# Kernel optimization log

Hardware: AMD Instinct MI355X
Metric: run time of the kernel (lower is better)

## Reference

```python
import jax, jax.numpy as jnp
import numpy as np

HIDDEN = 1024
NUM_HEADS = 16
HEAD_SIZE = HIDDEN // NUM_HEADS


def setup_inputs() -> dict:
    key = jax.random.key(0)
    k1, k2, k3 = jax.random.split(key, 3)
    B, S = 2, 2048
    x = jax.random.normal(k1, (B, S, HIDDEN), dtype=jnp.float32)
    # query projection (source reuses it for both q and k)
    Wq = jax.random.normal(k2, (HIDDEN, HIDDEN), dtype=jnp.float32) / np.sqrt(HIDDEN)
    bq = jax.random.normal(k3, (HIDDEN,), dtype=jnp.float32) * 0.01
    return {"x": x, "Wq": Wq, "bq": bq}


def reference(x, Wq, bq):
    B, S, _ = x.shape
    # NOTE: source bug-for-bug: k uses the query projection too
    q = x @ Wq + bq                      # [B,S,D]
    k = x @ Wq + bq                      # [B,S,D]
    q = q.reshape(B, S, NUM_HEADS, HEAD_SIZE)
    k = k.reshape(B, S, NUM_HEADS, HEAD_SIZE)
    # scores: [B,H,S,S]
    e = jnp.einsum("bqhd,bkhd->bhqk", q, k)
    s = jax.nn.softmax(e / jnp.sqrt(jnp.float32(HEAD_SIZE)), axis=-1)
    return s
```

## Files before the change

### kernel.cpp

```cpp
#include <hip/hip_runtime.h>

#define HIDDEN 1024
#define SEQ 2048
#define NB 2
#define PSTRIDE 2052
#define NT 16

typedef _Float16 half8 __attribute__((ext_vector_type(8)));
typedef _Float16 half4 __attribute__((ext_vector_type(4)));
typedef float f32x4 __attribute__((ext_vector_type(4)));

#define GL2LDS(gp, lp) __builtin_amdgcn_global_load_lds( \
    (const __attribute__((address_space(1))) void*)(gp), \
    (__attribute__((address_space(3))) void*)(lp), 16, 0, 0)

__global__ __launch_bounds__(256) void cast_wt(const float* __restrict__ w,
                                               _Float16* __restrict__ wt) {
    __shared__ float tile[32][33];
    int bx = blockIdx.x * 32, by = blockIdx.y * 32;
    int tx = threadIdx.x, ty = threadIdx.y;
    #pragma unroll
    for (int i = 0; i < 32; i += 8)
        tile[ty + i][tx] = w[(by + ty + i) * HIDDEN + bx + tx];
    __syncthreads();
    #pragma unroll
    for (int i = 0; i < 32; i += 8)
        wt[(bx + ty + i) * HIDDEN + by + tx] = (_Float16)tile[tx][ty + i];
}

__global__ __launch_bounds__(512) void proj_gemm(const float* __restrict__ X,
                                                 const _Float16* __restrict__ Bt,
                                                 const float* __restrict__ bias,
                                                 _Float16* __restrict__ Q) {
    __shared__ _Float16 As[128 * 64];
    __shared__ _Float16 Bs[128 * 64];
    const int m0 = blockIdx.x * 128;
    const int n0 = blockIdx.y * 128;
    const int tid = threadIdx.x;
    const int w = tid >> 6, l = tid & 63;
    const int wm = w >> 2, wn = w & 3;
    const int lrow = l & 15, lkslot = l >> 4;

    const int srow = l >> 3, sslot = l & 7;

    f32x4 acc[4][2] = {};

    for (int k0 = 0; k0 < HIDDEN; k0 += 64) {
        __syncthreads();
        #pragma unroll
        for (int j = 0; j < 2; ++j) {
            const int chunk = w * 2 + j;
            const int r = chunk * 8 + srow;
            const int gslot = sslot ^ (r & 7);
            GL2LDS(&Bt[(size_t)(n0 + r) * HIDDEN + k0 + gslot * 8], Bs + chunk * 512);
        }
        #pragma unroll
        for (int it = 0; it < 2; ++it) {
            const int id = it * 512 + tid;
            const int row = id >> 3, slot = id & 7;
            const float* src = &X[(size_t)(m0 + row) * HIDDEN + k0 + slot * 8];
            f32x4 v0 = *(const f32x4*)src;
            f32x4 v1 = *(const f32x4*)(src + 4);
            half8 hv;
            hv[0] = (_Float16)v0[0]; hv[1] = (_Float16)v0[1];
            hv[2] = (_Float16)v0[2]; hv[3] = (_Float16)v0[3];
            hv[4] = (_Float16)v1[0]; hv[5] = (_Float16)v1[1];
            hv[6] = (_Float16)v1[2]; hv[7] = (_Float16)v1[3];
            *(half8*)&As[row * 64 + (slot ^ (row & 7)) * 8] = hv;
        }
        __syncthreads();
        #pragma unroll
        for (int kk = 0; kk < 64; kk += 32) {
            const int csb = kk >> 3;
            half8 af[4], bf[2];
            #pragma unroll
            for (int m = 0; m < 4; ++m) {
                const int R = wm * 64 + m * 16 + lrow;
                const int slot = (csb + lkslot) ^ (R & 7);
                af[m] = *(const half8*)&As[R * 64 + slot * 8];
            }
            #pragma unroll
            for (int n = 0; n < 2; ++n) {
                const int R = wn * 32 + n * 16 + lrow;
                const int slot = (csb + lkslot) ^ (R & 7);
                bf[n] = *(const half8*)&Bs[R * 64 + slot * 8];
            }
            #pragma unroll
            for (int m = 0; m < 4; ++m)
                #pragma unroll
                for (int n = 0; n < 2; ++n)
                    acc[m][n] = __builtin_amdgcn_mfma_f32_16x16x32_f16(af[m], bf[n], acc[m][n], 0, 0, 0);
        }
    }
    const int lr4 = (l >> 4) * 4, lc = l & 15;
    #pragma unroll
    for (int n = 0; n < 2; ++n) {
        int gcol = n0 + wn * 32 + n * 16 + lc;
        float b = bias[gcol];
        #pragma unroll
        for (int m = 0; m < 4; ++m) {
            #pragma unroll
            for (int r = 0; r < 4; ++r) {
                int grow = m0 + wm * 64 + m * 16 + lr4 + r;
                Q[(size_t)grow * HIDDEN + gcol] = (_Float16)(acc[m][n][r] + b);
            }
        }
    }
}

__global__ __launch_bounds__(1024, 4) void scores_softmax(const _Float16* __restrict__ Qh,
                                                          float* __restrict__ out) {
    __shared__ __align__(16) _Float16 p[2][16][PSTRIDE];
    __shared__ float rsum_lds[2][8][16];

    const int raw = blockIdx.x;
    const int xcd = raw & 7, i = raw >> 3;
    const int bh = xcd * 4 + (i >> 3);
    const int qchunk = i & 7;
    const int b = bh >> 4, h = bh & 15;

    const int tid = threadIdx.x;
    const int wv = tid >> 6;
    const int l = tid & 63;
    const int lq = l & 15, lg = l >> 4;
    const int hoff = h * 64;
    const _Float16* qbase = Qh + (size_t)b * SEQ * HIDDEN;
    const size_t outbase = (size_t)(b * 16 + h) * SEQ * SEQ;

    if (wv < 8) {
        const int pw = wv;
        const _Float16* kbase = qbase + (size_t)(pw * 256 + lq) * HIDDEN + hoff + lg * 8;
        for (int t = 0; t <= NT; ++t) {
            if (t < NT) {
                const int buf = t & 1;
                const int q0 = qchunk * 256 + t * 16;
                const _Float16* qp = qbase + (size_t)(q0 + lq) * HIDDEN + hoff + lg * 8;
                const half8 bq0 = *(const half8*)qp;
                const half8 bq1 = *(const half8*)(qp + 32);
                float rsum = 0.f;
                #pragma unroll
                for (int s = 0; s < 16; ++s) {
                    const _Float16* a = kbase + (size_t)s * 16 * HIDDEN;
                    half8 ka = *(const half8*)a;
                    half8 kb = *(const half8*)(a + 32);
                    f32x4 acc = {};
                    acc = __builtin_amdgcn_mfma_f32_16x16x32_f16(ka, bq0, acc, 0, 0, 0);
                    acc = __builtin_amdgcn_mfma_f32_16x16x32_f16(kb, bq1, acc, 0, 0, 0);
                    float e0 = exp2f(fmaf(acc[0], 0.18033688011f, -11.54156033f));
                    float e1 = exp2f(fmaf(acc[1], 0.18033688011f, -11.54156033f));
                    float e2 = exp2f(fmaf(acc[2], 0.18033688011f, -11.54156033f));
                    float e3 = exp2f(fmaf(acc[3], 0.18033688011f, -11.54156033f));
                    rsum += (e0 + e1) + (e2 + e3);
                    half4 hv;
                    hv[0] = (_Float16)e0; hv[1] = (_Float16)e1;
                    hv[2] = (_Float16)e2; hv[3] = (_Float16)e3;
                    *(half4*)&p[buf][lq][pw * 256 + s * 16 + lg * 4] = hv;
                }
                rsum += __shfl_xor(rsum, 16);
                rsum += __shfl_xor(rsum, 32);
                if (l < 16) rsum_lds[buf][pw][l] = rsum;
            }
            asm volatile("s_waitcnt lgkmcnt(0)" ::: "memory");
            __builtin_amdgcn_s_barrier();
        }
    } else {
        const int cw = wv - 8;
        for (int t = 0; t <= NT; ++t) {
            if (t > 0) {
                const int pbuf = (t - 1) & 1;
                #pragma unroll
                for (int rr = 0; rr < 2; ++rr) {
                    const int r = cw * 2 + rr;
                    float rs = 0.f;
                    #pragma unroll
                    for (int w8 = 0; w8 < 8; ++w8) rs += rsum_lds[pbuf][w8][r];
                    const float rinv = 1.0f / rs;
                    float* orow = out + outbase
                                + (size_t)(qchunk * 256 + (t - 1) * 16 + r) * SEQ;
                    #pragma unroll
                    for (int ii = 0; ii < 8; ++ii) {
                        half4 hv = *(const half4*)&p[pbuf][r][ii * 256 + l * 4];
                        f32x4 v;
                        v[0] = (float)hv[0] * rinv; v[1] = (float)hv[1] * rinv;
                        v[2] = (float)hv[2] * rinv; v[3] = (float)hv[3] * rinv;
                        __builtin_nontemporal_store(v, (f32x4*)(orow + ii * 256 + l * 4));
                    }
                }
            }
            asm volatile("s_waitcnt lgkmcnt(0)" ::: "memory");
            __builtin_amdgcn_s_barrier();
        }
    }
}

extern "C" void kernel_launch(void* const* d_in, const int* in_sizes, int n_in,
                              void* d_out, int out_size, void* d_ws, size_t ws_size,
                              hipStream_t stream) {
    const float* x  = (const float*)d_in[0];
    const float* Wq = (const float*)d_in[1];
    const float* bq = (const float*)d_in[2];
    float* out = (float*)d_out;

    _Float16* qh = (_Float16*)d_ws;
    _Float16* wt = qh + (size_t)4 * 1024 * 1024;

    cast_wt<<<dim3(32, 32), dim3(32, 8), 0, stream>>>(Wq, wt);
    proj_gemm<<<dim3(NB * SEQ / 128, HIDDEN / 128), 512, 0, stream>>>(x, wt, bq, qh);
    scores_softmax<<<256, 1024, 0, stream>>>(qh, out);
}
```

Baseline: 131.4 us.

## Double-buffer projection GEMM tiles and remap blocks for XCD-local reuse

The projection GEMM now keeps two LDS buffers for its A and B tiles. The next k-slice is fetched into registers (X) and LDS (W via global_load_lds) while MFMAs run on the current slice, so global load latency overlaps compute and there is one barrier per iteration instead of two. The grid is flattened to 256 blocks, and the block index is remapped so blocks on the same XCD share M tiles and reuse X in L2. The cost is double the LDS and extra live registers for the prefetched fp32 X values.

```diff
diff --git a/kernel.cpp b/kernel.cpp
--- a/kernel.cpp
+++ b/kernel.cpp
@@ -32,10 +32,13 @@
                                                  const _Float16* __restrict__ Bt,
                                                  const float* __restrict__ bias,
                                                  _Float16* __restrict__ Q) {
-    __shared__ _Float16 As[128 * 64];
-    __shared__ _Float16 Bs[128 * 64];
-    const int m0 = blockIdx.x * 128;
-    const int n0 = blockIdx.y * 128;
+    __shared__ _Float16 As[2][128 * 64];
+    __shared__ _Float16 Bs[2][128 * 64];
+    const int raw = blockIdx.x;
+    const int xcd = raw & 7, j = raw >> 3;
+    const int mt = xcd * 4 + (j >> 3);
+    const int ntile = j & 7;
+    const int m0 = mt * 128, n0 = ntile * 128;
     const int tid = threadIdx.x;
     const int w = tid >> 6, l = tid & 63;
     const int wm = w >> 2, wn = w & 3;
@@ -43,32 +46,60 @@
 
     const int srow = l >> 3, sslot = l & 7;
 
+    f32x4 av[2][2];
+
     f32x4 acc[4][2] = {};
 
-    for (int k0 = 0; k0 < HIDDEN; k0 += 64) {
-        __syncthreads();
-        #pragma unroll
-        for (int j = 0; j < 2; ++j) {
-            const int chunk = w * 2 + j;
+    {
+        #pragma unroll
+        for (int j2 = 0; j2 < 2; ++j2) {
+            const int chunk = w * 2 + j2;
             const int r = chunk * 8 + srow;
             const int gslot = sslot ^ (r & 7);
-            GL2LDS(&Bt[(size_t)(n0 + r) * HIDDEN + k0 + gslot * 8], Bs + chunk * 512);
+            GL2LDS(&Bt[(size_t)(n0 + r) * HIDDEN + gslot * 8], &Bs[0][chunk * 512]);
         }
         #pragma unroll
         for (int it = 0; it < 2; ++it) {
             const int id = it * 512 + tid;
             const int row = id >> 3, slot = id & 7;
-            const float* src = &X[(size_t)(m0 + row) * HIDDEN + k0 + slot * 8];
-            f32x4 v0 = *(const f32x4*)src;
-            f32x4 v1 = *(const f32x4*)(src + 4);
+            const float* src = &X[(size_t)(m0 + row) * HIDDEN + slot * 8];
+            av[it][0] = *(const f32x4*)src;
+            av[it][1] = *(const f32x4*)(src + 4);
+        }
+        #pragma unroll
+        for (int it = 0; it < 2; ++it) {
+            const int id = it * 512 + tid;
+            const int row = id >> 3, slot = id & 7;
             half8 hv;
-            hv[0] = (_Float16)v0[0]; hv[1] = (_Float16)v0[1];
-            hv[2] = (_Float16)v0[2]; hv[3] = (_Float16)v0[3];
-            hv[4] = (_Float16)v1[0]; hv[5] = (_Float16)v1[1];
-            hv[6] = (_Float16)v1[2]; hv[7] = (_Float16)v1[3];
-            *(half8*)&As[row * 64 + (slot ^ (row & 7)) * 8] = hv;
+            hv[0] = (_Float16)av[it][0][0]; hv[1] = (_Float16)av[it][0][1];
+            hv[2] = (_Float16)av[it][0][2]; hv[3] = (_Float16)av[it][0][3];
+            hv[4] = (_Float16)av[it][1][0]; hv[5] = (_Float16)av[it][1][1];
+            hv[6] = (_Float16)av[it][1][2]; hv[7] = (_Float16)av[it][1][3];
+            *(half8*)&As[0][row * 64 + (slot ^ (row & 7)) * 8] = hv;
         }
         __syncthreads();
+    }
+
+    for (int t = 0; t < 16; ++t) {
+        const int cur = t & 1, nxt = cur ^ 1;
+        const int k1 = (t + 1) * 64;
+        if (t < 15) {
+            #pragma unroll
+            for (int j2 = 0; j2 < 2; ++j2) {
+                const int chunk = w * 2 + j2;
+                const int r = chunk * 8 + srow;
+                const int gslot = sslot ^ (r & 7);
+                GL2LDS(&Bt[(size_t)(n0 + r) * HIDDEN + k1 + gslot * 8], &Bs[nxt][chunk * 512]);
+            }
+            #pragma unroll
+            for (int it = 0; it < 2; ++it) {
+                const int id = it * 512 + tid;
+                const int row = id >> 3, slot = id & 7;
+                const float* src = &X[(size_t)(m0 + row) * HIDDEN + k1 + slot * 8];
+                av[it][0] = *(const f32x4*)src;
+                av[it][1] = *(const f32x4*)(src + 4);
+            }
+        }
         #pragma unroll
         for (int kk = 0; kk < 64; kk += 32) {
             const int csb = kk >> 3;
@@ -77,13 +108,13 @@
             for (int m = 0; m < 4; ++m) {
                 const int R = wm * 64 + m * 16 + lrow;
                 const int slot = (csb + lkslot) ^ (R & 7);
-                af[m] = *(const half8*)&As[R * 64 + slot * 8];
+                af[m] = *(const half8*)&As[cur][R * 64 + slot * 8];
             }
             #pragma unroll
             for (int n = 0; n < 2; ++n) {
                 const int R = wn * 32 + n * 16 + lrow;
                 const int slot = (csb + lkslot) ^ (R & 7);
-                bf[n] = *(const half8*)&Bs[R * 64 + slot * 8];
+                bf[n] = *(const half8*)&Bs[cur][R * 64 + slot * 8];
             }
             #pragma unroll
             for (int m = 0; m < 4; ++m)
@@ -91,7 +122,22 @@
                 for (int n = 0; n < 2; ++n)
                     acc[m][n] = __builtin_amdgcn_mfma_f32_16x16x32_f16(af[m], bf[n], acc[m][n], 0, 0, 0);
         }
-    }
+        if (t < 15) {
+            #pragma unroll
+            for (int it = 0; it < 2; ++it) {
+                const int id = it * 512 + tid;
+                const int row = id >> 3, slot = id & 7;
+                half8 hv;
+                hv[0] = (_Float16)av[it][0][0]; hv[1] = (_Float16)av[it][0][1];
+                hv[2] = (_Float16)av[it][0][2]; hv[3] = (_Float16)av[it][0][3];
+                hv[4] = (_Float16)av[it][1][0]; hv[5] = (_Float16)av[it][1][1];
+                hv[6] = (_Float16)av[it][1][2]; hv[7] = (_Float16)av[it][1][3];
+                *(half8*)&As[nxt][row * 64 + (slot ^ (row & 7)) * 8] = hv;
+            }
+        }
+        __syncthreads();
+    }
+
     const int lr4 = (l >> 4) * 4, lc = l & 15;
     #pragma unroll
     for (int n = 0; n < 2; ++n) {
@@ -205,6 +251,6 @@
     _Float16* wt = qh + (size_t)4 * 1024 * 1024;
 
     cast_wt<<<dim3(32, 32), dim3(32, 8), 0, stream>>>(Wq, wt);
-    proj_gemm<<<dim3(NB * SEQ / 128, HIDDEN / 128), 512, 0, stream>>>(x, wt, bq, qh);
+    proj_gemm<<<256, 512, 0, stream>>>(x, wt, bq, qh);
     scores_softmax<<<256, 1024, 0, stream>>>(qh, out);
 }
```

Result: no change. 133.1 us (+1.3%).

## Replace producer/consumer LDS softmax with register-resident per-block scores

Applied to the files above, without the earlier changes.

The scores/softmax kernel drops the warp-specialized producer/consumer scheme, where 8 waves computed exp scores into a double-buffered LDS tile and 8 other waves normalized and stored them. Each 256-thread block now handles 16 query rows. Each wave keeps its 512 columns of fp16 exponentials in registers and software-prefetches the next K fragment. Row sums are combined through a tiny LDS array with a single barrier. This removes the large LDS footprint and the per-tile barriers, and gives many more small blocks for occupancy, at the cost of high register pressure (32 half4 values per thread) and no overlap between computing scores and storing them within a block.

```diff
diff --git a/kernel.cpp b/kernel.cpp
--- a/kernel.cpp
+++ b/kernel.cpp
@@ -3,8 +3,6 @@
 #define HIDDEN 1024
 #define SEQ 2048
 #define NB 2
-#define PSTRIDE 2052
-#define NT 16
 
 typedef _Float16 half8 __attribute__((ext_vector_type(8)));
 typedef _Float16 half4 __attribute__((ext_vector_type(4)));
@@ -108,88 +106,74 @@
     }
 }
 
-__global__ __launch_bounds__(1024, 4) void scores_softmax(const _Float16* __restrict__ Qh,
-                                                          float* __restrict__ out) {
-    __shared__ __align__(16) _Float16 p[2][16][PSTRIDE];
-    __shared__ float rsum_lds[2][8][16];
+__global__ __launch_bounds__(256) void scores_softmax(const _Float16* __restrict__ Qh,
+                                                      float* __restrict__ out) {
+    __shared__ float rsum_lds[4][16];
 
     const int raw = blockIdx.x;
-    const int xcd = raw & 7, i = raw >> 3;
-    const int bh = xcd * 4 + (i >> 3);
-    const int qchunk = i & 7;
+    const int bid = (raw & 7) * 512 + (raw >> 3);
+    const int bh = bid >> 7;
+    const int qb = bid & 127;
     const int b = bh >> 4, h = bh & 15;
 
     const int tid = threadIdx.x;
-    const int wv = tid >> 6;
+    const int w = tid >> 6;
     const int l = tid & 63;
     const int lq = l & 15, lg = l >> 4;
+    const int q0 = qb * 16;
     const int hoff = h * 64;
     const _Float16* qbase = Qh + (size_t)b * SEQ * HIDDEN;
-    const size_t outbase = (size_t)(b * 16 + h) * SEQ * SEQ;
 
-    if (wv < 8) {
-        const int pw = wv;
-        const _Float16* kbase = qbase + (size_t)(pw * 256 + lq) * HIDDEN + hoff + lg * 8;
-        for (int t = 0; t <= NT; ++t) {
-            if (t < NT) {
-                const int buf = t & 1;
-                const int q0 = qchunk * 256 + t * 16;
-                const _Float16* qp = qbase + (size_t)(q0 + lq) * HIDDEN + hoff + lg * 8;
-                const half8 bq0 = *(const half8*)qp;
-                const half8 bq1 = *(const half8*)(qp + 32);
-                float rsum = 0.f;
-                #pragma unroll
-                for (int s = 0; s < 16; ++s) {
-                    const _Float16* a = kbase + (size_t)s * 16 * HIDDEN;
-                    half8 ka = *(const half8*)a;
-                    half8 kb = *(const half8*)(a + 32);
-                    f32x4 acc = {};
-                    acc = __builtin_amdgcn_mfma_f32_16x16x32_f16(ka, bq0, acc, 0, 0, 0);
-                    acc = __builtin_amdgcn_mfma_f32_16x16x32_f16(kb, bq1, acc, 0, 0, 0);
-                    float e0 = exp2f(fmaf(acc[0], 0.18033688011f, -11.54156033f));
-                    float e1 = exp2f(fmaf(acc[1], 0.18033688011f, -11.54156033f));
-                    float e2 = exp2f(fmaf(acc[2], 0.18033688011f, -11.54156033f));
-                    float e3 = exp2f(fmaf(acc[3], 0.18033688011f, -11.54156033f));
-                    rsum += (e0 + e1) + (e2 + e3);
-                    half4 hv;
-                    hv[0] = (_Float16)e0; hv[1] = (_Float16)e1;
-                    hv[2] = (_Float16)e2; hv[3] = (_Float16)e3;
-                    *(half4*)&p[buf][lq][pw * 256 + s * 16 + lg * 4] = hv;
-                }
-                rsum += __shfl_xor(rsum, 16);
-                rsum += __shfl_xor(rsum, 32);
-                if (l < 16) rsum_lds[buf][pw][l] = rsum;
-            }
-            asm volatile("s_waitcnt lgkmcnt(0)" ::: "memory");
-            __builtin_amdgcn_s_barrier();
-        }
-    } else {
-        const int cw = wv - 8;
-        for (int t = 0; t <= NT; ++t) {
-            if (t > 0) {
-                const int pbuf = (t - 1) & 1;
-                #pragma unroll
-                for (int rr = 0; rr < 2; ++rr) {
-                    const int r = cw * 2 + rr;
-                    float rs = 0.f;
-                    #pragma unroll
-                    for (int w8 = 0; w8 < 8; ++w8) rs += rsum_lds[pbuf][w8][r];
-                    const float rinv = 1.0f / rs;
-                    float* orow = out + outbase
-                                + (size_t)(qchunk * 256 + (t - 1) * 16 + r) * SEQ;
-                    #pragma unroll
-                    for (int ii = 0; ii < 8; ++ii) {
-                        half4 hv = *(const half4*)&p[pbuf][r][ii * 256 + l * 4];
-                        f32x4 v;
-                        v[0] = (float)hv[0] * rinv; v[1] = (float)hv[1] * rinv;
-                        v[2] = (float)hv[2] * rinv; v[3] = (float)hv[3] * rinv;
-                        __builtin_nontemporal_store(v, (f32x4*)(orow + ii * 256 + l * 4));
-                    }
-                }
-            }
-            asm volatile("s_waitcnt lgkmcnt(0)" ::: "memory");
-            __builtin_amdgcn_s_barrier();
-        }
+    const _Float16* qp = qbase + (size_t)(q0 + lq) * HIDDEN + hoff + lg * 8;
+    const half8 bq0 = *(const half8*)qp;
+    const half8 bq1 = *(const half8*)(qp + 32);
+
+    const _Float16* kbase = qbase + (size_t)(w * 512 + lq) * HIDDEN + hoff + lg * 8;
+
+    half4 pv[32];
+    float rsum = 0.f;
+
+    half8 ka = *(const half8*)kbase;
+    half8 kb = *(const half8*)(kbase + 32);
+    #pragma unroll
+    for (int s = 0; s < 32; ++s) {
+        const int sn = (s < 31) ? s + 1 : 0;
+        const _Float16* a = kbase + (size_t)sn * 16 * HIDDEN;
+        half8 na = *(const half8*)a;
+        half8 nb = *(const half8*)(a + 32);
+
+        f32x4 acc = {};
+        acc = __builtin_amdgcn_mfma_f32_16x16x32_f16(ka, bq0, acc, 0, 0, 0);
+        acc = __builtin_amdgcn_mfma_f32_16x16x32_f16(kb, bq1, acc, 0, 0, 0);
+        float e0 = exp2f(fmaf(acc[0], 0.18033688011f, -11.54156033f));
+        float e1 = exp2f(fmaf(acc[1], 0.18033688011f, -11.54156033f));
+        float e2 = exp2f(fmaf(acc[2], 0.18033688011f, -11.54156033f));
+        float e3 = exp2f(fmaf(acc[3], 0.18033688011f, -11.54156033f));
+        rsum += (e0 + e1) + (e2 + e3);
+        half4 hv;
+        hv[0] = (_Float16)e0; hv[1] = (_Float16)e1;
+        hv[2] = (_Float16)e2; hv[3] = (_Float16)e3;
+        pv[s] = hv;
+        ka = na; kb = nb;
+    }
+
+    rsum += __shfl_xor(rsum, 16);
+    rsum += __shfl_xor(rsum, 32);
+    if (l < 16) rsum_lds[w][l] = rsum;
+    __syncthreads();
+    const float rs = rsum_lds[0][lq] + rsum_lds[1][lq] + rsum_lds[2][lq] + rsum_lds[3][lq];
+    const float rinv = 1.0f / rs;
+
+    float* orow = out + (size_t)(b * 16 + h) * SEQ * SEQ
+                      + (size_t)(q0 + lq) * SEQ + w * 512 + lg * 4;
+    #pragma unroll
+    for (int s = 0; s < 32; ++s) {
+        f32x4 v;
+        v[0] = (float)pv[s][0] * rinv;
+        v[1] = (float)pv[s][1] * rinv;
+        v[2] = (float)pv[s][2] * rinv;
+        v[3] = (float)pv[s][3] * rinv;
+        __builtin_nontemporal_store(v, (f32x4*)(orow + s * 16));
     }
 }
 
@@ -206,5 +190,5 @@
 
     cast_wt<<<dim3(32, 32), dim3(32, 8), 0, stream>>>(Wq, wt);
     proj_gemm<<<dim3(NB * SEQ / 128, HIDDEN / 128), 512, 0, stream>>>(x, wt, bq, qh);
-    scores_softmax<<<256, 1024, 0, stream>>>(qh, out);
+    scores_softmax<<<NB * 16 * (SEQ / 16), 256, 0, stream>>>(qh, out);
 }
```

New measurement: 259.5 us. 1.97x slower.

## Unify producer/consumer waves and keep K fragments resident in registers

Applied to the files above, without the earlier changes.

The kernel no longer splits into 8 score-computing waves and 8 store waves. All 16 waves now compute scores for a 128-key slice and then each normalizes and streams out one query row, with one barrier per tile. Each wave's K fragments are loaded once into registers and reused across all 16 query tiles, which removes the repeated global K loads, and the next Q tile is prefetched after the barrier. The trade is that compute and stores no longer overlap across waves, register pressure rises without the occupancy hint, and one buffer could be overwritten early since only a single barrier separates writes of buf from the reads two iterations later.

```diff
diff --git a/kernel.cpp b/kernel.cpp
--- a/kernel.cpp
+++ b/kernel.cpp
@@ -108,10 +108,10 @@
     }
 }
 
-__global__ __launch_bounds__(1024, 4) void scores_softmax(const _Float16* __restrict__ Qh,
-                                                          float* __restrict__ out) {
+__global__ __launch_bounds__(1024) void scores_softmax(const _Float16* __restrict__ Qh,
+                                                       float* __restrict__ out) {
     __shared__ __align__(16) _Float16 p[2][16][PSTRIDE];
-    __shared__ float rsum_lds[2][8][16];
+    __shared__ float rsum_lds[2][16][16];
 
     const int raw = blockIdx.x;
     const int xcd = raw & 7, i = raw >> 3;
@@ -127,68 +127,64 @@
     const _Float16* qbase = Qh + (size_t)b * SEQ * HIDDEN;
     const size_t outbase = (size_t)(b * 16 + h) * SEQ * SEQ;
 
-    if (wv < 8) {
-        const int pw = wv;
-        const _Float16* kbase = qbase + (size_t)(pw * 256 + lq) * HIDDEN + hoff + lg * 8;
-        for (int t = 0; t <= NT; ++t) {
-            if (t < NT) {
-                const int buf = t & 1;
-                const int q0 = qchunk * 256 + t * 16;
-                const _Float16* qp = qbase + (size_t)(q0 + lq) * HIDDEN + hoff + lg * 8;
-                const half8 bq0 = *(const half8*)qp;
-                const half8 bq1 = *(const half8*)(qp + 32);
-                float rsum = 0.f;
-                #pragma unroll
-                for (int s = 0; s < 16; ++s) {
-                    const _Float16* a = kbase + (size_t)s * 16 * HIDDEN;
-                    half8 ka = *(const half8*)a;
-                    half8 kb = *(const half8*)(a + 32);
-                    f32x4 acc = {};
-                    acc = __builtin_amdgcn_mfma_f32_16x16x32_f16(ka, bq0, acc, 0, 0, 0);
-                    acc = __builtin_amdgcn_mfma_f32_16x16x32_f16(kb, bq1, acc, 0, 0, 0);
-                    float e0 = exp2f(fmaf(acc[0], 0.18033688011f, -11.54156033f));
-                    float e1 = exp2f(fmaf(acc[1], 0.18033688011f, -11.54156033f));
-                    float e2 = exp2f(fmaf(acc[2], 0.18033688011f, -11.54156033f));
-                    float e3 = exp2f(fmaf(acc[3], 0.18033688011f, -11.54156033f));
-                    rsum += (e0 + e1) + (e2 + e3);
-                    half4 hv;
-                    hv[0] = (_Float16)e0; hv[1] = (_Float16)e1;
-                    hv[2] = (_Float16)e2; hv[3] = (_Float16)e3;
-                    *(half4*)&p[buf][lq][pw * 256 + s * 16 + lg * 4] = hv;
-                }
-                rsum += __shfl_xor(rsum, 16);
-                rsum += __shfl_xor(rsum, 32);
-                if (l < 16) rsum_lds[buf][pw][l] = rsum;
-            }
-            asm volatile("s_waitcnt lgkmcnt(0)" ::: "memory");
-            __builtin_amdgcn_s_barrier();
-        }
-    } else {
-        const int cw = wv - 8;
-        for (int t = 0; t <= NT; ++t) {
-            if (t > 0) {
-                const int pbuf = (t - 1) & 1;
-                #pragma unroll
-                for (int rr = 0; rr < 2; ++rr) {
-                    const int r = cw * 2 + rr;
-                    float rs = 0.f;
-                    #pragma unroll
-                    for (int w8 = 0; w8 < 8; ++w8) rs += rsum_lds[pbuf][w8][r];
-                    const float rinv = 1.0f / rs;
-                    float* orow = out + outbase
-                                + (size_t)(qchunk * 256 + (t - 1) * 16 + r) * SEQ;
-                    #pragma unroll
-                    for (int ii = 0; ii < 8; ++ii) {
-                        half4 hv = *(const half4*)&p[pbuf][r][ii * 256 + l * 4];
-                        f32x4 v;
-                        v[0] = (float)hv[0] * rinv; v[1] = (float)hv[1] * rinv;
-                        v[2] = (float)hv[2] * rinv; v[3] = (float)hv[3] * rinv;
-                        __builtin_nontemporal_store(v, (f32x4*)(orow + ii * 256 + l * 4));
-                    }
-                }
-            }
-            asm volatile("s_waitcnt lgkmcnt(0)" ::: "memory");
-            __builtin_amdgcn_s_barrier();
+    half8 ka[8], kb[8];
+    {
+        const _Float16* kbase = qbase + (size_t)(wv * 128 + lq) * HIDDEN + hoff + lg * 8;
+        #pragma unroll
+        for (int s = 0; s < 8; ++s) {
+            const _Float16* a = kbase + (size_t)s * 16 * HIDDEN;
+            ka[s] = *(const half8*)a;
+            kb[s] = *(const half8*)(a + 32);
+        }
+    }
+    const _Float16* qrow0 = qbase + (size_t)(qchunk * 256 + lq) * HIDDEN + hoff + lg * 8;
+    half8 q0 = *(const half8*)qrow0;
+    half8 q1 = *(const half8*)(qrow0 + 32);
+
+    for (int t = 0; t < NT; ++t) {
+        const int buf = t & 1;
+        float rsum = 0.f;
+        #pragma unroll
+        for (int s = 0; s < 8; ++s) {
+            f32x4 acc = {};
+            acc = __builtin_amdgcn_mfma_f32_16x16x32_f16(ka[s], q0, acc, 0, 0, 0);
+            acc = __builtin_amdgcn_mfma_f32_16x16x32_f16(kb[s], q1, acc, 0, 0, 0);
+            float e0 = exp2f(fmaf(acc[0], 0.18033688011f, -11.54156033f));
+            float e1 = exp2f(fmaf(acc[1], 0.18033688011f, -11.54156033f));
+            float e2 = exp2f(fmaf(acc[2], 0.18033688011f, -11.54156033f));
+            float e3 = exp2f(fmaf(acc[3], 0.18033688011f, -11.54156033f));
+            rsum += (e0 + e1) + (e2 + e3);
+            half4 hv;
+            hv[0] = (_Float16)e0; hv[1] = (_Float16)e1;
+            hv[2] = (_Float16)e2; hv[3] = (_Float16)e3;
+            *(half4*)&p[buf][lq][wv * 128 + s * 16 + lg * 4] = hv;
+        }
+        rsum += __shfl_xor(rsum, 16);
+        rsum += __shfl_xor(rsum, 32);
+        if (l < 16) rsum_lds[buf][wv][l] = rsum;
+
+        asm volatile("s_waitcnt lgkmcnt(0)" ::: "memory");
+        __builtin_amdgcn_s_barrier();
+
+        if (t + 1 < NT) {
+            const _Float16* qp = qbase + (size_t)(qchunk * 256 + (t + 1) * 16 + lq) * HIDDEN
+                               + hoff + lg * 8;
+            q0 = *(const half8*)qp;
+            q1 = *(const half8*)(qp + 32);
+        }
+
+        float rs = 0.f;
+        #pragma unroll
+        for (int w8 = 0; w8 < 16; ++w8) rs += rsum_lds[buf][w8][wv];
+        const float rinv = 1.0f / rs;
+        float* orow = out + outbase + (size_t)(qchunk * 256 + t * 16 + wv) * SEQ;
+        #pragma unroll
+        for (int ii = 0; ii < 8; ++ii) {
+            half4 hv = *(const half4*)&p[buf][wv][ii * 256 + l * 4];
+            f32x4 v;
+            v[0] = (float)hv[0] * rinv; v[1] = (float)hv[1] * rinv;
+            v[2] = (float)hv[2] * rinv; v[3] = (float)hv[3] * rinv;
+            __builtin_nontemporal_store(v, (f32x4*)(orow + ii * 256 + l * 4));
         }
     }
 }
```

Measured after the change: 137.2 us. +4.4%, slower.
